# Performance work log

Hardware: AMD Instinct MI355X
Metric: run time of the kernel (lower is better)

Reference implementation:

```python
import jax, jax.numpy as jnp
import numpy as np

N_NODES = 100000
N_EDGES = 1_600_000
D_EMB = 64
D_HID = 128


def setup_inputs() -> dict:
    key = jax.random.key(0)
    k1, k2, k3, k4 = jax.random.split(key, 4)
    emb = jax.random.normal(k1, (N_NODES, D_EMB), dtype=jnp.float32)
    W1 = jax.random.normal(k2, (D_EMB, D_HID), dtype=jnp.float32) * 0.05
    b1 = jnp.zeros((D_HID,), dtype=jnp.float32)
    W2 = jax.random.normal(k3, (D_HID, D_EMB), dtype=jnp.float32) * 0.05
    b2 = jnp.zeros((D_EMB,), dtype=jnp.float32)
    edge_index = jax.random.randint(k4, (2, N_EDGES), 0, N_NODES, dtype=jnp.int64 if jax.config.jax_enable_x64 else jnp.int32)
    return {"emb": emb, "W1": W1, "b1": b1, "W2": W2, "b2": b2,
            "edge_index": edge_index, "num_nodes": N_NODES}


def _gcn_conv(x, W, b, src, dst, deg_inv_sqrt, num_nodes):
    # PyG GCNConv: linear transform, then normalized scatter-add aggregation.
    x = x @ W                                   # [N, out]
    norm = deg_inv_sqrt[src] * deg_inv_sqrt[dst]  # [E+N]
    msg = x[src] * norm[:, None]                # gather + scale
    out = jax.ops.segment_sum(msg, dst, num_segments=num_nodes)
    return out + b


def reference(emb, W1, b1, W2, b2, edge_index, num_nodes):
    # Add self-loops (PyG GCNConv default add_self_loops=True).
    loops = jnp.arange(num_nodes, dtype=edge_index.dtype)
    src = jnp.concatenate([edge_index[0], loops])
    dst = jnp.concatenate([edge_index[1], loops])
    # Symmetric normalization degree (computed on destination, incl. loops).
    deg = jax.ops.segment_sum(jnp.ones(src.shape, dtype=emb.dtype), dst,
                              num_segments=num_nodes)
    dinv = jnp.where(deg > 0, jax.lax.rsqrt(jnp.maximum(deg, 1e-12)), 0.0)

    x = _gcn_conv(emb, W1, b1, src, dst, dinv, num_nodes)
    x = jax.nn.relu(x)
    x = _gcn_conv(x, W2, b2, src, dst, dinv, num_nodes)
    return x
```

## Files before the change

kernel.cpp:

```cpp
#include <hip/hip_runtime.h>


constexpr int D_EMB = 64;
constexpr int D_HID = 128;
constexpr int CB_LOG = 9;
constexpr int CB = 1 << CB_LOG;
constexpr int CAP = 16384;
constexpr int FB_EPT = 16;
constexpr int FB_CHUNK = 256 * FB_EPT;

__device__ inline unsigned int f2bf1(float f) {
    unsigned int u = __float_as_uint(f);
    return (u + 0x7FFFu + ((u >> 16) & 1u)) >> 16;
}
__device__ inline float blo(unsigned int u) { return __uint_as_float(u << 16); }
__device__ inline float bhi(unsigned int u) { return __uint_as_float(u & 0xFFFF0000u); }

__global__ __launch_bounds__(256) void k_f2bf(const float* __restrict__ in,
                                              uint4* __restrict__ out, int n8) {
    int i = blockIdx.x * 256 + threadIdx.x;
    int stride = gridDim.x * 256;
    for (; i < n8; i += stride) {
        float4 a = ((const float4*)in)[i * 2];
        float4 b = ((const float4*)in)[i * 2 + 1];
        uint4 o;
        o.x = f2bf1(a.x) | (f2bf1(a.y) << 16);
        o.y = f2bf1(a.z) | (f2bf1(a.w) << 16);
        o.z = f2bf1(b.x) | (f2bf1(b.y) << 16);
        o.w = f2bf1(b.z) | (f2bf1(b.w) << 16);
        out[i] = o;
    }
}

__global__ __launch_bounds__(256) void k_binit(int* __restrict__ bcur) {
    bcur[threadIdx.x * 16] = threadIdx.x * CAP;
}

__global__ __launch_bounds__(256) void k_fillb(const int* __restrict__ ei,
                                               int* __restrict__ bcur,
                                               unsigned int* __restrict__ recs, int E) {
    __shared__ int hist[4][256];
    __shared__ int lcur[256];
    const int tid  = threadIdx.x;
    const int w    = tid >> 6;
    const int base = blockIdx.x * FB_CHUNK;

    for (int i = tid; i < 4 * 256; i += 256) ((int*)hist)[i] = 0;
    __syncthreads();

    int s[FB_EPT], d[FB_EPT];
#pragma unroll
    for (int i = 0; i < FB_EPT; ++i) {
        int e = base + tid + i * 256;
        if (e < E) {
            s[i] = ei[e];
            d[i] = ei[E + e];
            atomicAdd(&hist[w][d[i] >> CB_LOG], 1);
        } else {
            d[i] = -1;
        }
    }
    __syncthreads();

    int h = hist[0][tid] + hist[1][tid] + hist[2][tid] + hist[3][tid];
    if (h > 0) lcur[tid] = atomicAdd(&bcur[tid * 16], h);
    __syncthreads();

#pragma unroll
    for (int i = 0; i < FB_EPT; ++i) {
        if (d[i] >= 0) {
            int b   = d[i] >> CB_LOG;
            int pos = atomicAdd(&lcur[b], 1);
            recs[pos] = ((unsigned int)(d[i] & (CB - 1)) << 23) | (unsigned int)s[i];
        }
    }
}

__global__ __launch_bounds__(256) void k_bscan(const int* __restrict__ bcur,
                                               int* __restrict__ bbase,
                                               int* __restrict__ row_ptr,
                                               int nbuckc, int N, int E) {
    __shared__ int ts[256];
    const int tid = threadIdx.x;
    int s = (tid < nbuckc) ? (bcur[tid * 16] - tid * CAP) : 0;
    ts[tid] = s;
    __syncthreads();
    for (int off = 1; off < 256; off <<= 1) {
        int t = (tid >= off) ? ts[tid - off] : 0;
        __syncthreads();
        ts[tid] += t;
        __syncthreads();
    }
    if (tid < nbuckc) bbase[tid] = ts[tid] - s;
    if (tid == nbuckc - 1) bbase[nbuckc] = ts[tid];
    if (tid == 0) row_ptr[N] = E;
}

__global__ __launch_bounds__(1024) void k_binsort(const unsigned int* __restrict__ recs,
                                                  const int* __restrict__ bbase,
                                                  int* __restrict__ row_ptr,
                                                  float* __restrict__ dinv,
                                                  unsigned int* __restrict__ srcs, int N) {
    __shared__ int ld[CB];
    const int b   = blockIdx.x;
    const int n0  = b * CB;
    const int tid = threadIdx.x;
    const int nn  = min(CB, N - n0);
    const int obeg = bbase[b];
    const int sz   = bbase[b + 1] - obeg;
    const unsigned int* rb = recs + (size_t)b * CAP;

    if (tid < nn) ld[tid] = 0;
    __syncthreads();

    for (int i = tid; i < sz; i += 1024)
        atomicAdd(&ld[rb[i] >> 23], 1);
    __syncthreads();

    int own = (tid < nn) ? ld[tid] : 0;
    for (int off = 1; off < CB; off <<= 1) {
        int t = (tid >= off && tid < nn) ? ld[tid - off] : 0;
        __syncthreads();
        if (tid < nn) ld[tid] += t;
        __syncthreads();
    }
    int incl = (tid < nn) ? ld[tid] : 0;
    __syncthreads();
    if (tid < nn) {
        int rp = obeg + incl - own;
        row_ptr[n0 + tid] = rp;
        dinv[n0 + tid] = rsqrtf((float)(own + 1));
        ld[tid] = rp;
    }
    __syncthreads();

    for (int i = tid; i < sz; i += 1024) {
        unsigned int rec = rb[i];
        int pos = atomicAdd(&ld[rec >> 23], 1);
        srcs[pos] = rec & 0x7FFFFF;
    }
}

template <int K, int OUT, int BM, bool BIAS, bool RELU, bool OUTBF>
__global__ __launch_bounds__(256) void k_gemm(
    const float* __restrict__ A, const float* __restrict__ W,
    const float* __restrict__ bias, void* __restrict__ Xout, int N) {
    constexpr int NCG = OUT / 4;
    constexpr int NRG = 256 / NCG;
    constexpr int RPT = BM / NRG;

    __shared__ float As[BM][K + 1];
    __shared__ float Ws[K][OUT];

    const int tid  = threadIdx.x;
    const int row0 = blockIdx.x * BM;

    for (int i = tid; i < K * OUT / 4; i += 256)
        ((float4*)Ws)[i] = ((const float4*)W)[i];

    for (int i = tid; i < BM * K / 4; i += 256) {
        int r  = i / (K / 4);
        int k4 = i % (K / 4);
        int row = row0 + r;
        float4 v = make_float4(0.f, 0.f, 0.f, 0.f);
        if (row < N) v = ((const float4*)(A + (size_t)row * K))[k4];
        As[r][k4 * 4 + 0] = v.x;
        As[r][k4 * 4 + 1] = v.y;
        As[r][k4 * 4 + 2] = v.z;
        As[r][k4 * 4 + 3] = v.w;
    }
    __syncthreads();

    const int tc = tid % NCG;
    const int tr = tid / NCG;
    const int r0 = tr * RPT;

    float acc[RPT][4];
#pragma unroll
    for (int i = 0; i < RPT; ++i)
        acc[i][0] = acc[i][1] = acc[i][2] = acc[i][3] = 0.f;

#pragma unroll 8
    for (int k = 0; k < K; ++k) {
        float4 w = *(const float4*)&Ws[k][tc * 4];
#pragma unroll
        for (int i = 0; i < RPT; ++i) {
            float a = As[r0 + i][k];
            acc[i][0] = fmaf(a, w.x, acc[i][0]);
            acc[i][1] = fmaf(a, w.y, acc[i][1]);
            acc[i][2] = fmaf(a, w.z, acc[i][2]);
            acc[i][3] = fmaf(a, w.w, acc[i][3]);
        }
    }

    float4 bb = make_float4(0.f, 0.f, 0.f, 0.f);
    if (BIAS) bb = ((const float4*)bias)[tc];

#pragma unroll
    for (int i = 0; i < RPT; ++i) {
        int row = row0 + r0 + i;
        if (row >= N) break;
        float4 v = make_float4(acc[i][0], acc[i][1], acc[i][2], acc[i][3]);
        if (BIAS) { v.x += bb.x; v.y += bb.y; v.z += bb.z; v.w += bb.w; }
        if (RELU) {
            v.x = fmaxf(v.x, 0.f); v.y = fmaxf(v.y, 0.f);
            v.z = fmaxf(v.z, 0.f); v.w = fmaxf(v.w, 0.f);
        }
        if (OUTBF) {
            unsigned int* Xb = (unsigned int*)Xout;
            uint2 p;
            p.x = f2bf1(v.x) | (f2bf1(v.y) << 16);
            p.y = f2bf1(v.z) | (f2bf1(v.w) << 16);
            ((uint2*)(Xb + (size_t)row * (OUT / 2)))[tc] = p;
        } else {
            ((float4*)((float*)Xout + (size_t)row * OUT))[tc] = v;
        }
    }
}

template <bool BIAS>
__global__ __launch_bounds__(256) void k_gather64b(
    const int* __restrict__ row_ptr, const unsigned int* __restrict__ srcs,
    const float* __restrict__ dinv, const unsigned int* __restrict__ Xb,
    const float* __restrict__ bias, float* __restrict__ OUT, int N) {
    const int wid  = (blockIdx.x * 256 + threadIdx.x) >> 6;
    const int lane = threadIdx.x & 63;
    const int g    = lane >> 3;
    const int l    = lane & 7;
    if (wid >= N) return;
    const int v = wid;
    const float dv = dinv[v];
    const int beg = row_ptr[v];
    const int end = row_ptr[v + 1];

    float acc[8];
#pragma unroll
    for (int i = 0; i < 8; ++i) acc[i] = 0.f;

    int j = beg + g;
    int s = (j < end) ? (int)srcs[j] : -1;
    while (s >= 0) {
        int jn = j + 8;
        int sn = (jn < end) ? (int)srcs[jn] : -1;
        float w = dinv[s] * dv;
        uint4 xb = ((const uint4*)(Xb + (size_t)s * 32))[l];
        acc[0] = fmaf(blo(xb.x), w, acc[0]); acc[1] = fmaf(bhi(xb.x), w, acc[1]);
        acc[2] = fmaf(blo(xb.y), w, acc[2]); acc[3] = fmaf(bhi(xb.y), w, acc[3]);
        acc[4] = fmaf(blo(xb.z), w, acc[4]); acc[5] = fmaf(bhi(xb.z), w, acc[5]);
        acc[6] = fmaf(blo(xb.w), w, acc[6]); acc[7] = fmaf(bhi(xb.w), w, acc[7]);
        s = sn; j = jn;
    }

#pragma unroll
    for (int m = 8; m <= 32; m <<= 1) {
#pragma unroll
        for (int i = 0; i < 8; ++i) acc[i] += __shfl_xor(acc[i], m);
    }

    if (g == 0) {
        uint4 xb = ((const uint4*)(Xb + (size_t)v * 32))[l];
        float s2 = dv * dv;
        acc[0] = fmaf(blo(xb.x), s2, acc[0]); acc[1] = fmaf(bhi(xb.x), s2, acc[1]);
        acc[2] = fmaf(blo(xb.y), s2, acc[2]); acc[3] = fmaf(bhi(xb.y), s2, acc[3]);
        acc[4] = fmaf(blo(xb.z), s2, acc[4]); acc[5] = fmaf(bhi(xb.z), s2, acc[5]);
        acc[6] = fmaf(blo(xb.w), s2, acc[6]); acc[7] = fmaf(bhi(xb.w), s2, acc[7]);
        if (BIAS) {
            float4 b0 = ((const float4*)bias)[l * 2];
            float4 b1 = ((const float4*)bias)[l * 2 + 1];
            acc[0] += b0.x; acc[1] += b0.y; acc[2] += b0.z; acc[3] += b0.w;
            acc[4] += b1.x; acc[5] += b1.y; acc[6] += b1.z; acc[7] += b1.w;
        }
        float* orow = OUT + (size_t)v * 64;
        ((float4*)orow)[l * 2]     = make_float4(acc[0], acc[1], acc[2], acc[3]);
        ((float4*)orow)[l * 2 + 1] = make_float4(acc[4], acc[5], acc[6], acc[7]);
    }
}

extern "C" void kernel_launch(void* const* d_in, const int* in_sizes, int n_in,
                              void* d_out, int out_size, void* d_ws, size_t ws_size,
                              hipStream_t stream) {
    const float* emb = (const float*)d_in[0];
    const float* W1  = (const float*)d_in[1];
    const float* b1  = (const float*)d_in[2];
    const float* W2  = (const float*)d_in[3];
    const float* b2  = (const float*)d_in[4];
    const int*   ei  = (const int*)d_in[5];

    const int N = in_sizes[0] / D_EMB;
    const int E = in_sizes[5] / 2;
    const int nbuckc = (N + CB - 1) / CB;

    float*        a1      = (float*)d_ws;
    float*        h1      = a1 + (size_t)N * D_EMB;
    unsigned int* srcs    = (unsigned int*)(h1 + (size_t)N * D_HID);
    unsigned int* recs    = srcs + E;
    int*          row_ptr = (int*)(recs + (size_t)nbuckc * CAP);
    int*          bcur    = row_ptr + (N + 1);
    int*          bbase   = bcur + 256 * 16;
    float*        dinv    = (float*)(bbase + 257);
    unsigned int* embb    = (unsigned int*)(dinv + N);
    unsigned int* x2b     = (unsigned int*)a1;
    float*        out     = (float*)d_out;

    const int nbFb  = (E + FB_CHUNK - 1) / FB_CHUNK;
    const int nbGat = (N * 64 + 255) / 256;

    k_f2bf<<<2048, 256, 0, stream>>>(emb, (uint4*)embb, N * D_EMB / 8);

    k_binit<<<1, 256, 0, stream>>>(bcur);
    k_fillb<<<nbFb, 256, 0, stream>>>(ei, bcur, recs, E);
    k_bscan<<<1, 256, 0, stream>>>(bcur, bbase, row_ptr, nbuckc, N, E);
    k_binsort<<<nbuckc, 1024, 0, stream>>>(recs, bbase, row_ptr, dinv, srcs, N);

    k_gather64b<false><<<nbGat, 256, 0, stream>>>(row_ptr, srcs, dinv, embb, nullptr, a1, N);
    k_gemm<D_EMB, D_HID, 64, true, true, false><<<(N + 63) / 64, 256, 0, stream>>>(a1, W1, b1, h1, N);

    k_gemm<D_HID, D_EMB, 32, false, false, true><<<(N + 31) / 32, 256, 0, stream>>>(h1, W2, nullptr, x2b, N);
    k_gather64b<true><<<nbGat, 256, 0, stream>>>(row_ptr, srcs, dinv, x2b, b2, out, N);
}
```

Measured before the change: 291.9 us.

## Pre-scale features by dinv and gather from feature-sliced bf16 layout

Source features are pre-multiplied by dinv[src] before bf16 packing, which removes the per-edge dinv gather and multiply in the aggregation. Features are stored in eight 16-byte column slices laid out slice-major, so each gather block reads one slice whose table (1.6 MB) is small enough to stay cache-resident. The new aggregation kernel has 16 lanes per node per slice and applies dinv[dst] once at the end. The trade-off is more blocks and each edge index being read once per slice, plus an extra rounding step because the dinv scaling now happens before bf16 conversion.

After: 381.4 us. 30.6% more time.

```diff
diff --git a/kernel.cpp b/kernel.cpp
--- a/kernel.cpp
+++ b/kernel.cpp
@@ -8,29 +8,15 @@
 constexpr int CAP = 16384;
 constexpr int FB_EPT = 16;
 constexpr int FB_CHUNK = 256 * FB_EPT;
-
-__device__ inline unsigned int f2bf1(float f) {
-    unsigned int u = __float_as_uint(f);
+constexpr int NSLICE = 8;
+constexpr int DPS = 8;
+
+__device__ inline unsigned f2bf1(float f) {
+    unsigned u = __float_as_uint(f);
     return (u + 0x7FFFu + ((u >> 16) & 1u)) >> 16;
 }
-__device__ inline float blo(unsigned int u) { return __uint_as_float(u << 16); }
-__device__ inline float bhi(unsigned int u) { return __uint_as_float(u & 0xFFFF0000u); }
-
-__global__ __launch_bounds__(256) void k_f2bf(const float* __restrict__ in,
-                                              uint4* __restrict__ out, int n8) {
-    int i = blockIdx.x * 256 + threadIdx.x;
-    int stride = gridDim.x * 256;
-    for (; i < n8; i += stride) {
-        float4 a = ((const float4*)in)[i * 2];
-        float4 b = ((const float4*)in)[i * 2 + 1];
-        uint4 o;
-        o.x = f2bf1(a.x) | (f2bf1(a.y) << 16);
-        o.y = f2bf1(a.z) | (f2bf1(a.w) << 16);
-        o.z = f2bf1(b.x) | (f2bf1(b.y) << 16);
-        o.w = f2bf1(b.z) | (f2bf1(b.w) << 16);
-        out[i] = o;
-    }
-}
+__device__ inline float blo(unsigned u) { return __uint_as_float(u << 16); }
+__device__ inline float bhi(unsigned u) { return __uint_as_float(u & 0xFFFF0000u); }
 
 __global__ __launch_bounds__(256) void k_binit(int* __restrict__ bcur) {
     bcur[threadIdx.x * 16] = threadIdx.x * CAP;
@@ -141,10 +127,92 @@
     }
 }
 
+__global__ __launch_bounds__(256) void k_f2bfY(const float* __restrict__ X,
+                                               const float* __restrict__ dinv,
+                                               uint4* __restrict__ Ys, int N) {
+    int i = blockIdx.x * 256 + threadIdx.x;
+    int stride = gridDim.x * 256;
+    int total = N * NSLICE;
+    for (; i < total; i += stride) {
+        int node = i >> 3, s = i & 7;
+        float dv = dinv[node];
+        const float* src = X + (size_t)node * 64 + s * DPS;
+        float4 a = ((const float4*)src)[0];
+        float4 b = ((const float4*)src)[1];
+        uint4 o;
+        o.x = f2bf1(dv * a.x) | (f2bf1(dv * a.y) << 16);
+        o.y = f2bf1(dv * a.z) | (f2bf1(dv * a.w) << 16);
+        o.z = f2bf1(dv * b.x) | (f2bf1(dv * b.y) << 16);
+        o.w = f2bf1(dv * b.z) | (f2bf1(dv * b.w) << 16);
+        Ys[(size_t)s * N + node] = o;
+    }
+}
+
+template <bool BIAS>
+__global__ __launch_bounds__(256) void k_sgat(
+    const int* __restrict__ row_ptr, const unsigned int* __restrict__ srcs,
+    const uint4* __restrict__ Ys, const float* __restrict__ dinv,
+    const float* __restrict__ bias, float* __restrict__ OUT, int N) {
+    const int tid  = threadIdx.x;
+    const int l    = tid & 15;
+    const int q    = tid >> 4;
+    const int s    = blockIdx.x & (NSLICE - 1);
+    const int node = (blockIdx.x >> 3) * 16 + q;
+    if (node >= N) return;
+    const uint4* Yt = Ys + (size_t)s * N;
+    const int beg = row_ptr[node];
+    const int end = row_ptr[node + 1];
+
+    float a0 = 0.f, a1 = 0.f, a2 = 0.f, a3 = 0.f;
+    float a4 = 0.f, a5 = 0.f, a6 = 0.f, a7 = 0.f;
+
+    for (int j = beg + l; j < end; j += 16) {
+        uint4 y = Yt[srcs[j]];
+        a0 += blo(y.x); a1 += bhi(y.x);
+        a2 += blo(y.y); a3 += bhi(y.y);
+        a4 += blo(y.z); a5 += bhi(y.z);
+        a6 += blo(y.w); a7 += bhi(y.w);
+    }
+
+#pragma unroll
+    for (int m = 1; m <= 8; m <<= 1) {
+        a0 += __shfl_xor(a0, m); a1 += __shfl_xor(a1, m);
+        a2 += __shfl_xor(a2, m); a3 += __shfl_xor(a3, m);
+        a4 += __shfl_xor(a4, m); a5 += __shfl_xor(a5, m);
+        a6 += __shfl_xor(a6, m); a7 += __shfl_xor(a7, m);
+    }
+
+    if (l < 2) {
+        const float dv = dinv[node];
+        uint4 y = Yt[node];
+        float* orow = OUT + (size_t)node * 64 + s * DPS;
+        if (l == 0) {
+            a0 += blo(y.x); a1 += bhi(y.x);
+            a2 += blo(y.y); a3 += bhi(y.y);
+            float4 r = make_float4(dv * a0, dv * a1, dv * a2, dv * a3);
+            if (BIAS) {
+                r.x += bias[s * DPS + 0]; r.y += bias[s * DPS + 1];
+                r.z += bias[s * DPS + 2]; r.w += bias[s * DPS + 3];
+            }
+            ((float4*)orow)[0] = r;
+        } else {
+            a4 += blo(y.z); a5 += bhi(y.z);
+            a6 += blo(y.w); a7 += bhi(y.w);
+            float4 r = make_float4(dv * a4, dv * a5, dv * a6, dv * a7);
+            if (BIAS) {
+                r.x += bias[s * DPS + 4]; r.y += bias[s * DPS + 5];
+                r.z += bias[s * DPS + 6]; r.w += bias[s * DPS + 7];
+            }
+            ((float4*)orow)[1] = r;
+        }
+    }
+}
+
 template <int K, int OUT, int BM, bool BIAS, bool RELU, bool OUTBF>
 __global__ __launch_bounds__(256) void k_gemm(
     const float* __restrict__ A, const float* __restrict__ W,
-    const float* __restrict__ bias, void* __restrict__ Xout, int N) {
+    const float* __restrict__ bias, const float* __restrict__ dinv,
+    void* __restrict__ Xout, int N) {
     constexpr int NCG = OUT / 4;
     constexpr int NRG = 256 / NCG;
     constexpr int RPT = BM / NRG;
@@ -207,72 +275,17 @@
             v.z = fmaxf(v.z, 0.f); v.w = fmaxf(v.w, 0.f);
         }
         if (OUTBF) {
-            unsigned int* Xb = (unsigned int*)Xout;
+            float dvr = dinv[row];
+            v.x *= dvr; v.y *= dvr; v.z *= dvr; v.w *= dvr;
             uint2 p;
             p.x = f2bf1(v.x) | (f2bf1(v.y) << 16);
             p.y = f2bf1(v.z) | (f2bf1(v.w) << 16);
-            ((uint2*)(Xb + (size_t)row * (OUT / 2)))[tc] = p;
+            int sl = tc >> 1, half = tc & 1;
+            unsigned* Xb = (unsigned*)Xout;
+            *(uint2*)(Xb + ((size_t)sl * N + row) * 4 + half * 2) = p;
         } else {
             ((float4*)((float*)Xout + (size_t)row * OUT))[tc] = v;
         }
-    }
-}
-
-template <bool BIAS>
-__global__ __launch_bounds__(256) void k_gather64b(
-    const int* __restrict__ row_ptr, const unsigned int* __restrict__ srcs,
-    const float* __restrict__ dinv, const unsigned int* __restrict__ Xb,
-    const float* __restrict__ bias, float* __restrict__ OUT, int N) {
-    const int wid  = (blockIdx.x * 256 + threadIdx.x) >> 6;
-    const int lane = threadIdx.x & 63;
-    const int g    = lane >> 3;
-    const int l    = lane & 7;
-    if (wid >= N) return;
-    const int v = wid;
-    const float dv = dinv[v];
-    const int beg = row_ptr[v];
-    const int end = row_ptr[v + 1];
-
-    float acc[8];
-#pragma unroll
-    for (int i = 0; i < 8; ++i) acc[i] = 0.f;
-
-    int j = beg + g;
-    int s = (j < end) ? (int)srcs[j] : -1;
-    while (s >= 0) {
-        int jn = j + 8;
-        int sn = (jn < end) ? (int)srcs[jn] : -1;
-        float w = dinv[s] * dv;
-        uint4 xb = ((const uint4*)(Xb + (size_t)s * 32))[l];
-        acc[0] = fmaf(blo(xb.x), w, acc[0]); acc[1] = fmaf(bhi(xb.x), w, acc[1]);
-        acc[2] = fmaf(blo(xb.y), w, acc[2]); acc[3] = fmaf(bhi(xb.y), w, acc[3]);
-        acc[4] = fmaf(blo(xb.z), w, acc[4]); acc[5] = fmaf(bhi(xb.z), w, acc[5]);
-        acc[6] = fmaf(blo(xb.w), w, acc[6]); acc[7] = fmaf(bhi(xb.w), w, acc[7]);
-        s = sn; j = jn;
-    }
-
-#pragma unroll
-    for (int m = 8; m <= 32; m <<= 1) {
-#pragma unroll
-        for (int i = 0; i < 8; ++i) acc[i] += __shfl_xor(acc[i], m);
-    }
-
-    if (g == 0) {
-        uint4 xb = ((const uint4*)(Xb + (size_t)v * 32))[l];
-        float s2 = dv * dv;
-        acc[0] = fmaf(blo(xb.x), s2, acc[0]); acc[1] = fmaf(bhi(xb.x), s2, acc[1]);
-        acc[2] = fmaf(blo(xb.y), s2, acc[2]); acc[3] = fmaf(bhi(xb.y), s2, acc[3]);
-        acc[4] = fmaf(blo(xb.z), s2, acc[4]); acc[5] = fmaf(bhi(xb.z), s2, acc[5]);
-        acc[6] = fmaf(blo(xb.w), s2, acc[6]); acc[7] = fmaf(bhi(xb.w), s2, acc[7]);
-        if (BIAS) {
-            float4 b0 = ((const float4*)bias)[l * 2];
-            float4 b1 = ((const float4*)bias)[l * 2 + 1];
-            acc[0] += b0.x; acc[1] += b0.y; acc[2] += b0.z; acc[3] += b0.w;
-            acc[4] += b1.x; acc[5] += b1.y; acc[6] += b1.z; acc[7] += b1.w;
-        }
-        float* orow = OUT + (size_t)v * 64;
-        ((float4*)orow)[l * 2]     = make_float4(acc[0], acc[1], acc[2], acc[3]);
-        ((float4*)orow)[l * 2 + 1] = make_float4(acc[4], acc[5], acc[6], acc[7]);
     }
 }
 
@@ -292,29 +305,29 @@
 
     float*        a1      = (float*)d_ws;
     float*        h1      = a1 + (size_t)N * D_EMB;
-    unsigned int* srcs    = (unsigned int*)(h1 + (size_t)N * D_HID);
+    uint4*        Yb      = (uint4*)(h1 + (size_t)N * D_HID);
+    unsigned int* srcs    = (unsigned int*)(Yb + (size_t)NSLICE * N);
     unsigned int* recs    = srcs + E;
     int*          row_ptr = (int*)(recs + (size_t)nbuckc * CAP);
     int*          bcur    = row_ptr + (N + 1);
     int*          bbase   = bcur + 256 * 16;
     float*        dinv    = (float*)(bbase + 257);
-    unsigned int* embb    = (unsigned int*)(dinv + N);
-    unsigned int* x2b     = (unsigned int*)a1;
     float*        out     = (float*)d_out;
 
     const int nbFb  = (E + FB_CHUNK - 1) / FB_CHUNK;
-    const int nbGat = (N * 64 + 255) / 256;
-
-    k_f2bf<<<2048, 256, 0, stream>>>(emb, (uint4*)embb, N * D_EMB / 8);
+    const int nbSg  = ((N + 15) / 16) * NSLICE;
 
     k_binit<<<1, 256, 0, stream>>>(bcur);
     k_fillb<<<nbFb, 256, 0, stream>>>(ei, bcur, recs, E);
     k_bscan<<<1, 256, 0, stream>>>(bcur, bbase, row_ptr, nbuckc, N, E);
     k_binsort<<<nbuckc, 1024, 0, stream>>>(recs, bbase, row_ptr, dinv, srcs, N);
 
-    k_gather64b<false><<<nbGat, 256, 0, stream>>>(row_ptr, srcs, dinv, embb, nullptr, a1, N);
-    k_gemm<D_EMB, D_HID, 64, true, true, false><<<(N + 63) / 64, 256, 0, stream>>>(a1, W1, b1, h1, N);
-
-    k_gemm<D_HID, D_EMB, 32, false, false, true><<<(N + 31) / 32, 256, 0, stream>>>(h1, W2, nullptr, x2b, N);
-    k_gather64b<true><<<nbGat, 256, 0, stream>>>(row_ptr, srcs, dinv, x2b, b2, out, N);
-}
+    k_f2bfY<<<2048, 256, 0, stream>>>(emb, dinv, Yb, N);
+    k_sgat<false><<<nbSg, 256, 0, stream>>>(row_ptr, srcs, Yb, dinv, nullptr, a1, N);
+    k_gemm<D_EMB, D_HID, 64, true, true, false><<<(N + 63) / 64, 256, 0, stream>>>(
+        a1, W1, b1, nullptr, h1, N);
+
+    k_gemm<D_HID, D_EMB, 32, false, false, true><<<(N + 31) / 32, 256, 0, stream>>>(
+        h1, W2, nullptr, dinv, Yb, N);
+    k_sgat<true><<<nbSg, 256, 0, stream>>>(row_ptr, srcs, Yb, dinv, b2, out, N);
+}
```
